# Optimization experiments

Hardware: AMD Instinct MI355X
Metric: run time of the kernel (lower is better)

Reference implementation:

```python
import jax, jax.numpy as jnp
import numpy as np

N, E, F_IN, H, MH, C, G = 100000, 3200000, 128, 32, 64, 10, 64

def _seg_sum(data, ids, num):
    return jax.ops.segment_sum(data, ids, num_segments=num)

def gcn_conv(x, row, col, ew, W, b, n):
    # PyG GCNConv: linear first, then self-loops + symmetric edge-weight norm + scatter-add
    h = x @ W  # [N, H]
    loop = jnp.arange(n)
    r = jnp.concatenate([row, loop])
    c = jnp.concatenate([col, loop])
    w = jnp.concatenate([ew, jnp.ones((n,), dtype=ew.dtype)])
    deg = _seg_sum(w, c, n)
    dinv = jnp.where(deg > 0, jax.lax.rsqrt(deg), 0.0)
    norm = dinv[r] * w * dinv[c]  # [E+N]
    out = _seg_sum(norm[:, None] * h[r], c, n)  # scatter to targets
    return out + b

def setup_inputs():
    key = jax.random.key(0)
    ks = jax.random.split(key, 16)
    inp = {
        "x": jax.random.normal(ks[0], (N, F_IN), dtype=jnp.float32),
        "edge_index": jax.random.randint(ks[1], (2, E), 0, N, dtype=jnp.int64),
        "edge_weight": jax.random.uniform(ks[2], (E,), dtype=jnp.float32),
        "batch": jnp.sort(jax.random.randint(ks[3], (N,), 0, G, dtype=jnp.int64)),
    }
    def lin(k, i, o):
        s = 1.0 / np.sqrt(i)
        k1, k2 = jax.random.split(k)
        return (jax.random.uniform(k1, (i, o), minval=-s, maxval=s, dtype=jnp.float32),
                jax.random.uniform(k2, (o,), minval=-s, maxval=s, dtype=jnp.float32))
    inp["W1"], inp["b1"] = lin(ks[4], F_IN, H)
    inp["W2"], inp["b2"] = lin(ks[5], H, H)
    inp["W3"], inp["b3"] = lin(ks[6], H, H)
    inp["Wm0"], inp["bm0"] = lin(ks[7], H, MH)
    inp["Wm1"], inp["bm1"] = lin(ks[8], MH, MH)
    inp["Wout"], inp["bout"] = lin(ks[9], MH, C)
    return inp

def reference(x, edge_index, edge_weight, batch, W1, b1, W2, b2, W3, b3, Wm0, bm0, Wm1, bm1, Wout, bout):
    row, col = edge_index[0], edge_index[1]
    h = jax.nn.relu(gcn_conv(x, row, col, edge_weight, W1, b1, N))
    h = jax.nn.relu(gcn_conv(h, row, col, edge_weight, W2, b2, N))
    h = gcn_conv(h, row, col, edge_weight, W3, b3, N)
    # global mean pool over graphs
    sums = _seg_sum(h, batch, G)
    counts = _seg_sum(jnp.ones((N,), dtype=h.dtype), batch, G)
    g = sums / jnp.maximum(counts, 1.0)[:, None]
    # dropout p=0.5 is identity at inference (training=False)
    g = jax.nn.relu(g @ Wm0 + bm0)
    g = jax.nn.relu(g @ Wm1 + bm1)
    return g @ Wout + bout
```

## Files before the change

kernel.cpp:

```cpp
#include <hip/hip_runtime.h>

#define NN 100000
#define NE 3200000
#define FIN 128
#define HID 32
#define MH  64
#define NC  10
#define NG  64
#define NBKT 782
#define NBLK 512
#define EPB  (NE / NBLK)
#define SCANL (NBKT * NBLK)
#define SRCMASK 0x1FFFF
#define BCAP 5120

typedef float floatx2 __attribute__((ext_vector_type(2)));

__global__ __launch_bounds__(1024)
void hist_bkt(const int* __restrict__ ei, int* __restrict__ cnt2) {
    __shared__ int h[NBKT];
    int tid = threadIdx.x, blk = blockIdx.x;
    for (int b = tid; b < NBKT; b += 1024) h[b] = 0;
    __syncthreads();
    int base = blk * EPB;
    for (int i = tid; i < EPB; i += 1024)
        atomicAdd(&h[ei[NE + base + i] >> 7], 1);
    __syncthreads();
    for (int b = tid; b < NBKT; b += 1024) cnt2[b * NBLK + blk] = h[b];
}

__global__ void scan_block(const int* __restrict__ in, int* __restrict__ out,
                           int* __restrict__ bsum, int n) {
    __shared__ int lds[256];
    int tid = threadIdx.x;
    int base = blockIdx.x * 1024 + tid * 4;
    int v0 = 0, v1 = 0, v2 = 0, v3 = 0;
    if (base + 0 < n) v0 = in[base + 0];
    if (base + 1 < n) v1 = in[base + 1];
    if (base + 2 < n) v2 = in[base + 2];
    if (base + 3 < n) v3 = in[base + 3];
    int s = v0 + v1 + v2 + v3;
    lds[tid] = s;
    __syncthreads();
    for (int off = 1; off < 256; off <<= 1) {
        int val = (tid >= off) ? lds[tid - off] : 0;
        __syncthreads();
        lds[tid] += val;
        __syncthreads();
    }
    int excl = lds[tid] - s;
    if (tid == 255) bsum[blockIdx.x] = lds[255];
    if (base + 0 < n) out[base + 0] = excl;
    if (base + 1 < n) out[base + 1] = excl + v0;
    if (base + 2 < n) out[base + 2] = excl + v0 + v1;
    if (base + 3 < n) out[base + 3] = excl + v0 + v1 + v2;
}

__global__ void scan_top(int* __restrict__ bsum, int nb) {
    int lane = threadIdx.x;
    int carry = 0;
    for (int base = 0; base < nb; base += 64) {
        int i = base + lane;
        int orig = (i < nb) ? bsum[i] : 0;
        int v = orig;
#pragma unroll
        for (int off = 1; off < 64; off <<= 1) {
            int t = __shfl_up(v, off, 64);
            if (lane >= off) v += t;
        }
        if (i < nb) bsum[i] = carry + v - orig;
        carry += __shfl(v, 63, 64);
    }
}

__global__ void scan_add(int* __restrict__ data, const int* __restrict__ bsum, int n) {
    int i = blockIdx.x * 256 + threadIdx.x;
    if (i < n) data[i] += bsum[i >> 10];
}

__global__ __launch_bounds__(1024)
void scatter_bkt(const int* __restrict__ ei, const float* __restrict__ ew,
                 const int* __restrict__ cnt2, const int* __restrict__ scanned,
                 int2* __restrict__ tre) {
    __shared__ int2 pay[EPB];
    __shared__ int scur[NBKT];
    __shared__ int hexc[NBKT];
    __shared__ int gbase[NBKT];
    int tid = threadIdx.x, blk = blockIdx.x;
    int myh = 0;
    if (tid < NBKT) {
        myh = cnt2[tid * NBLK + blk];
        gbase[tid] = scanned[tid * NBLK + blk];
        scur[tid] = myh;
    }
    __syncthreads();
    for (int off = 1; off < NBKT; off <<= 1) {
        int v = (tid < NBKT && tid >= off) ? scur[tid - off] : 0;
        __syncthreads();
        if (tid < NBKT) scur[tid] += v;
        __syncthreads();
    }
    if (tid < NBKT) { int ex = scur[tid] - myh; hexc[tid] = ex; scur[tid] = ex; }
    __syncthreads();
    int base = blk * EPB;
    for (int i = tid; i < EPB; i += 1024) {
        int e = base + i;
        int c = ei[NE + e];
        int r = ei[e];
        unsigned int wb = __float_as_uint(ew[e]);
        int b = c >> 7;
        int j = atomicAdd(&scur[b], 1);
        pay[j] = make_int2(r | ((c & 127) << 17) | ((b & 0xFF) << 24),
                           (int)((wb & ~3u) | ((unsigned)b >> 8)));
    }
    __syncthreads();
    for (int j = tid; j < EPB; j += 1024) {
        int2 q = pay[j];
        int b = (int)((((unsigned)q.y & 3u) << 8) | (((unsigned)q.x >> 24) & 0xFFu));
        int pos = gbase[b] + (j - hexc[b]);
        tre[pos] = make_int2(q.x & 0x00FFFFFF, q.y & ~3);
    }
}

__global__ __launch_bounds__(512)
void sort_k(const int2* __restrict__ tre, const int* __restrict__ scanned,
            unsigned int* __restrict__ srn4, int* __restrict__ rowptr,
            float* __restrict__ dinv) {
    __shared__ int2 ed[BCAP];
    __shared__ int h[128];
    __shared__ float dw[128];
    __shared__ int sc[128];
    __shared__ int cur[128];
    int b = blockIdx.x, tid = threadIdx.x;
    int base = scanned[b * NBLK];
    int end = (b == NBKT - 1) ? NE : scanned[(b + 1) * NBLK];
    int n = end - base;
    bool staged = (n <= BCAP);
    if (tid < 128) { h[tid] = 0; dw[tid] = 0.f; }
    if (staged)
        for (int i = tid; i < n; i += 512) ed[i] = tre[base + i];
    __syncthreads();
    for (int i = tid; i < n; i += 512) {
        int2 q = staged ? ed[i] : tre[base + i];
        int key = (q.x >> 17) & 127;
        atomicAdd(&h[key], 1);
        atomicAdd(&dw[key], __int_as_float(q.y));
    }
    __syncthreads();
    if (tid < 128) sc[tid] = h[tid];
    __syncthreads();
    for (int off = 1; off < 128; off <<= 1) {
        int v = (tid < 128 && tid >= off) ? sc[tid - off] : 0;
        __syncthreads();
        if (tid < 128) sc[tid] += v;
        __syncthreads();
    }
    if (tid < 128) {
        int node = b * 128 + tid;
        if (node < NN) {
            rowptr[node] = base + sc[tid];
            dinv[node] = rsqrtf(1.0f + dw[tid]);
        }
        cur[tid] = base + sc[tid] - h[tid];
    }
    __syncthreads();
    for (int i = tid; i < n; i += 512) {
        int2 q = staged ? ed[i] : tre[base + i];
        int key = (q.x >> 17) & 127;
        int pos = atomicAdd(&cur[key], 1);
        unsigned int wb = (unsigned)q.y;
        wb += 0x7FFFu + ((wb >> 16) & 1u);
        srn4[pos] = (unsigned)(q.x & SRCMASK) | (((wb >> 16) & 0x7FFFu) << 17);
    }
}

template <int IN_DIM, bool RELU_IN>
__global__ __launch_bounds__(256)
void linear_k(const float* __restrict__ in, const float* __restrict__ W,
              const float* __restrict__ dinv, unsigned int* __restrict__ tmp8) {
    constexpr int J4 = IN_DIM / 4;
    constexpr int XSS = J4 + 1;
    __shared__ float4 xs[64 * XSS];
    __shared__ float4 wp[IN_DIM * 8];
    int tid = threadIdx.x;
    for (int idx = tid; idx < IN_DIM * 8; idx += 256) {
        int j = idx >> 3, kg = idx & 7;
        const float* wr = W + j * 32 + kg * 4;
        wp[idx] = make_float4(wr[0], wr[1], wr[2], wr[3]);
    }
    int rbase = blockIdx.x * 64;
    const float4* in4 = (const float4*)in;
    for (int idx = tid; idx < 64 * J4; idx += 256) {
        int row = idx / J4, j4 = idx % J4;
        int grow = rbase + row;
        float4 v = (grow < NN) ? in4[(size_t)grow * J4 + j4]
                               : make_float4(0.f, 0.f, 0.f, 0.f);
        if (RELU_IN) {
            v.x = fmaxf(v.x, 0.f); v.y = fmaxf(v.y, 0.f);
            v.z = fmaxf(v.z, 0.f); v.w = fmaxf(v.w, 0.f);
        }
        xs[row * XSS + j4] = v;
    }
    __syncthreads();
    int kg = tid & 7;
    int rp = tid >> 3;
    int r0 = rbase + 2 * rp;
    if (r0 >= NN) return;
    const float4* x0 = &xs[(2 * rp) * XSS];
    const float4* x1 = &xs[(2 * rp + 1) * XSS];
    float a00 = 0, a01 = 0, a02 = 0, a03 = 0;
    float a10 = 0, a11 = 0, a12 = 0, a13 = 0;
#pragma unroll
    for (int j4 = 0; j4 < J4; ++j4) {
        float4 v0 = x0[j4], v1 = x1[j4];
        const float4* wj = &wp[j4 * 4 * 8 + kg];
        float4 w0 = wj[0], w1 = wj[8], w2 = wj[16], w3 = wj[24];
#define LSTEP(VX0, VX1, W4) \
        a00 = fmaf(VX0, W4.x, a00); a01 = fmaf(VX0, W4.y, a01); \
        a02 = fmaf(VX0, W4.z, a02); a03 = fmaf(VX0, W4.w, a03); \
        a10 = fmaf(VX1, W4.x, a10); a11 = fmaf(VX1, W4.y, a11); \
        a12 = fmaf(VX1, W4.z, a12); a13 = fmaf(VX1, W4.w, a13);
        LSTEP(v0.x, v1.x, w0)
        LSTEP(v0.y, v1.y, w1)
        LSTEP(v0.z, v1.z, w2)
        LSTEP(v0.w, v1.w, w3)
#undef LSTEP
    }
    float d0 = dinv[r0], d1 = dinv[r0 + 1];
    a00 *= d0; a01 *= d0; a02 *= d0; a03 *= d0;
    a10 *= d1; a11 *= d1; a12 *= d1; a13 *= d1;
    int q0 = __builtin_amdgcn_cvt_pk_fp8_f32(a00, a01, 0, false);
    q0 = __builtin_amdgcn_cvt_pk_fp8_f32(a02, a03, q0, true);
    int q1 = __builtin_amdgcn_cvt_pk_fp8_f32(a10, a11, 0, false);
    q1 = __builtin_amdgcn_cvt_pk_fp8_f32(a12, a13, q1, true);
    tmp8[r0 * 8 + kg] = (unsigned int)q0;
    tmp8[(r0 + 1) * 8 + kg] = (unsigned int)q1;
}

__global__ void aggregate(const unsigned int* __restrict__ srn4,
                          const int* __restrict__ rowptr,
                          const float* __restrict__ dinv,
                          const float* __restrict__ bias,
                          const unsigned int* __restrict__ tmp8,
                          float* __restrict__ h) {
    int wid = (blockIdx.x * 256 + threadIdx.x) >> 6;
    if (wid >= NN) return;
    int lane = threadIdx.x & 63;
    int g = lane >> 3;
    int q = lane & 7;
    int end = rowptr[wid];
    int start = (wid == 0) ? 0 : rowptr[wid - 1];
    float a0 = 0, a1 = 0, a2 = 0, a3 = 0;
    float b0 = 0, b1 = 0, b2 = 0, b3 = 0;
    int e = start + g;
    for (; e + 24 < end; e += 32) {
        unsigned int p0 = srn4[e];
        unsigned int p1 = srn4[e + 8];
        unsigned int p2 = srn4[e + 16];
        unsigned int p3 = srn4[e + 24];
        unsigned int u0 = tmp8[(size_t)(p0 & SRCMASK) * 8 + q];
        unsigned int u1 = tmp8[(size_t)(p1 & SRCMASK) * 8 + q];
        unsigned int u2 = tmp8[(size_t)(p2 & SRCMASK) * 8 + q];
        unsigned int u3 = tmp8[(size_t)(p3 & SRCMASK) * 8 + q];
        float w0 = __uint_as_float((p0 >> 1) & 0x7FFF0000u);
        float w1 = __uint_as_float((p1 >> 1) & 0x7FFF0000u);
        float w2 = __uint_as_float((p2 >> 1) & 0x7FFF0000u);
        float w3 = __uint_as_float((p3 >> 1) & 0x7FFF0000u);
        floatx2 lo, hi;
        lo = __builtin_amdgcn_cvt_pk_f32_fp8(u0, false);
        hi = __builtin_amdgcn_cvt_pk_f32_fp8(u0, true);
        a0 = fmaf(w0, lo.x, a0); a1 = fmaf(w0, lo.y, a1);
        a2 = fmaf(w0, hi.x, a2); a3 = fmaf(w0, hi.y, a3);
        lo = __builtin_amdgcn_cvt_pk_f32_fp8(u1, false);
        hi = __builtin_amdgcn_cvt_pk_f32_fp8(u1, true);
        b0 = fmaf(w1, lo.x, b0); b1 = fmaf(w1, lo.y, b1);
        b2 = fmaf(w1, hi.x, b2); b3 = fmaf(w1, hi.y, b3);
        lo = __builtin_amdgcn_cvt_pk_f32_fp8(u2, false);
        hi = __builtin_amdgcn_cvt_pk_f32_fp8(u2, true);
        a0 = fmaf(w2, lo.x, a0); a1 = fmaf(w2, lo.y, a1);
        a2 = fmaf(w2, hi.x, a2); a3 = fmaf(w2, hi.y, a3);
        lo = __builtin_amdgcn_cvt_pk_f32_fp8(u3, false);
        hi = __builtin_amdgcn_cvt_pk_f32_fp8(u3, true);
        b0 = fmaf(w3, lo.x, b0); b1 = fmaf(w3, lo.y, b1);
        b2 = fmaf(w3, hi.x, b2); b3 = fmaf(w3, hi.y, b3);
    }
    for (; e < end; e += 8) {
        unsigned int p = srn4[e];
        unsigned int u = tmp8[(size_t)(p & SRCMASK) * 8 + q];
        float w = __uint_as_float((p >> 1) & 0x7FFF0000u);
        floatx2 lo = __builtin_amdgcn_cvt_pk_f32_fp8(u, false);
        floatx2 hi = __builtin_amdgcn_cvt_pk_f32_fp8(u, true);
        a0 = fmaf(w, lo.x, a0); a1 = fmaf(w, lo.y, a1);
        a2 = fmaf(w, hi.x, a2); a3 = fmaf(w, hi.y, a3);
    }
    a0 += b0; a1 += b1; a2 += b2; a3 += b3;
    a0 += __shfl_xor(a0, 8, 64); a1 += __shfl_xor(a1, 8, 64);
    a2 += __shfl_xor(a2, 8, 64); a3 += __shfl_xor(a3, 8, 64);
    a0 += __shfl_xor(a0, 16, 64); a1 += __shfl_xor(a1, 16, 64);
    a2 += __shfl_xor(a2, 16, 64); a3 += __shfl_xor(a3, 16, 64);
    a0 += __shfl_xor(a0, 32, 64); a1 += __shfl_xor(a1, 32, 64);
    a2 += __shfl_xor(a2, 32, 64); a3 += __shfl_xor(a3, 32, 64);
    if (g == 0) {
        float d = dinv[wid];
        unsigned int sv = tmp8[(size_t)wid * 8 + q];
        floatx2 slo = __builtin_amdgcn_cvt_pk_f32_fp8(sv, false);
        floatx2 shi = __builtin_amdgcn_cvt_pk_f32_fp8(sv, true);
        float4 bq = ((const float4*)bias)[q];
        float4 o;
        o.x = bq.x + d * (slo.x + a0);
        o.y = bq.y + d * (slo.y + a1);
        o.z = bq.z + d * (shi.x + a2);
        o.w = bq.w + d * (shi.y + a3);
        ((float4*)(h + (size_t)wid * HID))[q] = o;
    }
}

__global__ __launch_bounds__(256)
void pool_k(const float* __restrict__ h, const int* __restrict__ batch,
            float* __restrict__ sums, float* __restrict__ counts) {
    __shared__ float red[256];
    int g = blockIdx.x;
    int lo = 0, hi = NN;
    while (lo < hi) { int m = (lo + hi) >> 1; if (batch[m] < g) lo = m + 1; else hi = m; }
    int s = lo;
    lo = s; hi = NN;
    while (lo < hi) { int m = (lo + hi) >> 1; if (batch[m] < g + 1) lo = m + 1; else hi = m; }
    int e2 = lo;
    int tid = threadIdx.x;
    int r = tid >> 5, k = tid & 31;
    float acc = 0.f;
    for (int i = s + r; i < e2; i += 8) acc += h[(size_t)i * HID + k];
    red[tid] = acc;
    __syncthreads();
    for (int off = 128; off >= 32; off >>= 1) {
        if (tid < off) red[tid] += red[tid + off];
        __syncthreads();
    }
    if (tid < 32) sums[g * HID + tid] = red[tid];
    if (tid == 0) counts[g] = (float)(e2 - s);
}

__global__ __launch_bounds__(64)
void mlp_k(const float* __restrict__ sums, const float* __restrict__ counts,
           const float* __restrict__ Wm0, const float* __restrict__ bm0,
           const float* __restrict__ Wm1, const float* __restrict__ bm1,
           const float* __restrict__ Wout, const float* __restrict__ bout,
           float* __restrict__ out) {
    __shared__ float g0[HID];
    __shared__ float g1[MH];
    __shared__ float g2[MH];
    int g = blockIdx.x;
    int k = threadIdx.x;
    if (k < HID) g0[k] = sums[g * HID + k] / fmaxf(counts[g], 1.0f);
    __syncthreads();
    float acc = bm0[k];
#pragma unroll
    for (int j = 0; j < HID; ++j) acc = fmaf(g0[j], Wm0[j * MH + k], acc);
    g1[k] = fmaxf(acc, 0.f);
    __syncthreads();
    float acc2 = bm1[k];
#pragma unroll
    for (int j = 0; j < MH; ++j) acc2 = fmaf(g1[j], Wm1[j * MH + k], acc2);
    g2[k] = fmaxf(acc2, 0.f);
    __syncthreads();
    if (k < NC) {
        float acc3 = bout[k];
#pragma unroll
        for (int j = 0; j < MH; ++j) acc3 = fmaf(g2[j], Wout[j * NC + k], acc3);
        out[g * NC + k] = acc3;
    }
}

extern "C" void kernel_launch(void* const* d_in, const int* in_sizes, int n_in,
                              void* d_out, int out_size, void* d_ws, size_t ws_size,
                              hipStream_t stream) {
    const float* x    = (const float*)d_in[0];
    const int*   ei   = (const int*)d_in[1];
    const float* ew   = (const float*)d_in[2];
    const int*   batch= (const int*)d_in[3];
    const float* W1   = (const float*)d_in[4];
    const float* b1   = (const float*)d_in[5];
    const float* W2   = (const float*)d_in[6];
    const float* b2   = (const float*)d_in[7];
    const float* W3   = (const float*)d_in[8];
    const float* b3   = (const float*)d_in[9];
    const float* Wm0  = (const float*)d_in[10];
    const float* bm0  = (const float*)d_in[11];
    const float* Wm1  = (const float*)d_in[12];
    const float* bm1  = (const float*)d_in[13];
    const float* Wout = (const float*)d_in[14];
    const float* bout = (const float*)d_in[15];
    float* out = (float*)d_out;

    char* p = (char*)d_ws;
    unsigned int* srn4 = (unsigned int*)p; p += sizeof(unsigned int) * (size_t)NE;
    char*  S   = p;                      p += 12 * (size_t)NE;
    int2*  tre = (int2*)S;
    int*   cnt2    = (int*)(S + sizeof(int2) * (size_t)NE);
    int*   scanned = cnt2 + SCANL;
    unsigned int* tmp8 = (unsigned int*)S;
    float* hA  = (float*)(S + (size_t)NN * HID);
    float* hB  = hA + (size_t)NN * HID;
    int*   bsum    = (int*)p;            p += sizeof(int) * 512;
    float* dinv    = (float*)p;          p += sizeof(float) * NN;
    int*   rowptr  = (int*)p;            p += sizeof(int) * NN;
    float* sums    = (float*)p;          p += sizeof(float) * NG * HID;
    float* counts  = (float*)p;

    dim3 blk(256);
    const int NB_SCAN = (SCANL + 1023) / 1024;
    const int NB_LIN = (NN + 63) / 64;

    hist_bkt<<<NBLK, 1024, 0, stream>>>(ei, cnt2);
    scan_block<<<NB_SCAN, blk, 0, stream>>>(cnt2, scanned, bsum, SCANL);
    scan_top<<<1, 64, 0, stream>>>(bsum, NB_SCAN);
    scan_add<<<(SCANL + 255) / 256, blk, 0, stream>>>(scanned, bsum, SCANL);
    scatter_bkt<<<NBLK, 1024, 0, stream>>>(ei, ew, cnt2, scanned, tre);
    sort_k<<<NBKT, 512, 0, stream>>>(tre, scanned, srn4, rowptr, dinv);

    linear_k<FIN, false><<<NB_LIN, blk, 0, stream>>>(x, W1, dinv, tmp8);
    aggregate<<<25000, blk, 0, stream>>>(srn4, rowptr, dinv, b1, tmp8, hA);
    linear_k<HID, true><<<NB_LIN, blk, 0, stream>>>(hA, W2, dinv, tmp8);
    aggregate<<<25000, blk, 0, stream>>>(srn4, rowptr, dinv, b2, tmp8, hB);
    linear_k<HID, true><<<NB_LIN, blk, 0, stream>>>(hB, W3, dinv, tmp8);
    aggregate<<<25000, blk, 0, stream>>>(srn4, rowptr, dinv, b3, tmp8, hA);

    pool_k<<<NG, blk, 0, stream>>>(hA, batch, sums, counts);
    mlp_k<<<NG, 64, 0, stream>>>(sums, counts, Wm0, bm0, Wm1, bm1, Wout, bout, out);
}
```

Measured before the change: 441.3 us.

## Parallelize global mean pool over node chunks with atomic accumulation

After: 413.7 us. 1.07x faster.

```diff
diff --git a/kernel.cpp b/kernel.cpp
--- a/kernel.cpp
+++ b/kernel.cpp
@@ -56,8 +56,9 @@
     if (base + 3 < n) out[base + 3] = excl + v0 + v1 + v2;
 }
 
-__global__ void scan_top(int* __restrict__ bsum, int nb) {
+__global__ void scan_top(int* __restrict__ bsum, int nb, float* __restrict__ sc) {
     int lane = threadIdx.x;
+    for (int i = lane; i < NG * HID + NG; i += 64) sc[i] = 0.0f;
     int carry = 0;
     for (int base = 0; base < nb; base += 64) {
         int i = base + lane;
@@ -315,29 +316,27 @@
     }
 }
 
-__global__ __launch_bounds__(256)
-void pool_k(const float* __restrict__ h, const int* __restrict__ batch,
-            float* __restrict__ sums, float* __restrict__ counts) {
-    __shared__ float red[256];
-    int g = blockIdx.x;
-    int lo = 0, hi = NN;
-    while (lo < hi) { int m = (lo + hi) >> 1; if (batch[m] < g) lo = m + 1; else hi = m; }
-    int s = lo;
-    lo = s; hi = NN;
-    while (lo < hi) { int m = (lo + hi) >> 1; if (batch[m] < g + 1) lo = m + 1; else hi = m; }
-    int e2 = lo;
-    int tid = threadIdx.x;
-    int r = tid >> 5, k = tid & 31;
-    float acc = 0.f;
-    for (int i = s + r; i < e2; i += 8) acc += h[(size_t)i * HID + k];
-    red[tid] = acc;
-    __syncthreads();
-    for (int off = 128; off >= 32; off >>= 1) {
-        if (tid < off) red[tid] += red[tid + off];
-        __syncthreads();
-    }
-    if (tid < 32) sums[g * HID + tid] = red[tid];
-    if (tid == 0) counts[g] = (float)(e2 - s);
+__global__ void pool_k(const float* __restrict__ h, const int* __restrict__ batch,
+                       float* __restrict__ sums, float* __restrict__ counts) {
+    int t = blockIdx.x * 256 + threadIdx.x;
+    int chunk = t >> 5, k = t & 31;
+    int n0 = chunk * 32;
+    if (n0 >= NN) return;
+    int n1 = min(n0 + 32, NN);
+    int g = batch[n0];
+    float acc = 0.f, cacc = 0.f;
+    for (int i = n0; i < n1; ++i) {
+        int gi = batch[i];
+        if (gi != g) {
+            atomicAdd(&sums[g * HID + k], acc);
+            if (k == 0) atomicAdd(&counts[g], cacc);
+            g = gi; acc = 0.f; cacc = 0.f;
+        }
+        acc += h[(size_t)i * HID + k];
+        cacc += 1.f;
+    }
+    atomicAdd(&sums[g * HID + k], acc);
+    if (k == 0) atomicAdd(&counts[g], cacc);
 }
 
 __global__ __launch_bounds__(64)
@@ -413,7 +412,7 @@
 
     hist_bkt<<<NBLK, 1024, 0, stream>>>(ei, cnt2);
     scan_block<<<NB_SCAN, blk, 0, stream>>>(cnt2, scanned, bsum, SCANL);
-    scan_top<<<1, 64, 0, stream>>>(bsum, NB_SCAN);
+    scan_top<<<1, 64, 0, stream>>>(bsum, NB_SCAN, sums);
     scan_add<<<(SCANL + 255) / 256, blk, 0, stream>>>(scanned, bsum, SCANL);
     scatter_bkt<<<NBLK, 1024, 0, stream>>>(ei, ew, cnt2, scanned, tre);
     sort_k<<<NBKT, 512, 0, stream>>>(tre, scanned, srn4, rowptr, dinv);
@@ -425,6 +424,6 @@
     linear_k<HID, true><<<NB_LIN, blk, 0, stream>>>(hB, W3, dinv, tmp8);
     aggregate<<<25000, blk, 0, stream>>>(srn4, rowptr, dinv, b3, tmp8, hA);
 
-    pool_k<<<NG, blk, 0, stream>>>(hA, batch, sums, counts);
+    pool_k<<<391, blk, 0, stream>>>(hA, batch, sums, counts);
     mlp_k<<<NG, 64, 0, stream>>>(sums, counts, Wm0, bm0, Wm1, bm1, Wout, bout, out);
 }
```
